# Kernel optimization log

Measured on AMD Instinct MI355X. Metric: run time of the kernel, lower is better.

## Reference

```python
import jax, jax.numpy as jnp
import numpy as np
import math

N_EMBD = 384
N_HEAD = 6
HEAD_DIM = N_EMBD // N_HEAD  # 64
EPS = 1e-5


def apply_rotary_emb(x, cos, sin):
    # x: [B, T, H, D]; cos/sin: [1, T, 1, D//2]
    d = x.shape[3] // 2
    x1, x2 = x[..., :d], x[..., d:]
    y1 = x1 * cos + x2 * sin
    y2 = -x1 * sin + x2 * cos
    return jnp.concatenate([y1, y2], axis=3).astype(x.dtype)


def rms_norm(x):
    # no learned gain, eps inside the sqrt's argument as in the torch code
    return x * jax.lax.rsqrt(jnp.mean(x * x, axis=-1, keepdims=True) + EPS)


def setup_inputs() -> dict:
    key = jax.random.key(0)
    ks = jax.random.split(key, 7)
    B, T = 8, 2048
    x = jax.random.normal(ks[0], (B, T, N_EMBD), dtype=jnp.float32)
    scale = 1.0 / math.sqrt(N_EMBD)
    Wq = jax.random.normal(ks[1], (N_EMBD, N_EMBD), dtype=jnp.float32) * scale
    Wk = jax.random.normal(ks[2], (N_EMBD, N_EMBD), dtype=jnp.float32) * scale
    Wv = jax.random.normal(ks[3], (N_EMBD, N_EMBD), dtype=jnp.float32) * scale
    Wo = jax.random.normal(ks[4], (N_EMBD, N_EMBD), dtype=jnp.float32) * scale
    # RoPE tables: true cos/sin of position*inv_freq
    half = HEAD_DIM // 2
    inv_freq = 1.0 / (10000.0 ** (jnp.arange(half, dtype=jnp.float32) / half))
    t = jnp.arange(T, dtype=jnp.float32)
    freqs = t[:, None] * inv_freq[None, :]  # [T, half]
    cos = jnp.cos(freqs)[None, :, None, :]  # [1, T, 1, half]
    sin = jnp.sin(freqs)[None, :, None, :]
    return {"x": x, "Wq": Wq, "Wk": Wk, "Wv": Wv, "Wo": Wo, "cos": cos, "sin": sin}


def reference(x, Wq, Wk, Wv, Wo, cos, sin):
    B, T, C = x.shape
    H, D = N_HEAD, HEAD_DIM
    # torch Linear: y = x @ W.T (weights stored [out, in])
    q = (x @ Wq.T).reshape(B, T, H, D)
    k = (x @ Wk.T).reshape(B, T, H, D)
    v = (x @ Wv.T).reshape(B, T, H, D)
    q = apply_rotary_emb(q, cos, sin)
    k = apply_rotary_emb(k, cos, sin)
    q = rms_norm(q)
    k = rms_norm(k)
    # attention: [B, H, T, T] scores, full softmax (no causal mask in source)
    att = jnp.einsum("bthd,bshd->bhts", q, k) * (1.0 / math.sqrt(D))
    att = jax.nn.softmax(att, axis=-1)
    y = jnp.einsum("bhts,bshd->bthd", att, v).reshape(B, T, C)
    return y @ Wo.T
```

## Files before the change

kernel.cpp:

```cpp
#include <hip/hip_runtime.h>
#include <hip/hip_bf16.h>
#include <stdint.h>

#define B_ 8
#define T_ 2048
#define C_ 384
#define H_ 6
#define D_ 64
#define M_ (B_*T_)

typedef unsigned short u16;
typedef unsigned int u32;
typedef __attribute__((ext_vector_type(8))) short short8;
typedef __attribute__((ext_vector_type(4))) float floatx4;
typedef __attribute__((ext_vector_type(16))) float floatx16;

#define QSCALE 0.18033688011112042f

__device__ __forceinline__ u16 f2b(float f) {
  union { float f; unsigned u; } x; x.f = f;
  unsigned r = x.u + 0x7fffu + ((x.u >> 16) & 1u);
  return (u16)(r >> 16);
}
__device__ __forceinline__ u32 pack_bf16(float a, float b) {
  union { __hip_bfloat162 h; u32 u; } x;
  x.h = __float22bfloat162_rn(float2{a, b});
  return x.u;
}
__device__ __forceinline__ uint4 pack8(const float4& lo, const float4& hi) {
  uint4 r;
  r.x = pack_bf16(lo.x, lo.y); r.y = pack_bf16(lo.z, lo.w);
  r.z = pack_bf16(hi.x, hi.y); r.w = pack_bf16(hi.z, hi.w);
  return r;
}

__device__ __forceinline__ void plswap(u32& a, u32& b) {
  asm("v_permlane32_swap_b32 %0, %1" : "+v"(a), "+v"(b));
}

__device__ __forceinline__ float fexp2(float x) {
#if __has_builtin(__builtin_amdgcn_exp2f)
  return __builtin_amdgcn_exp2f(x);
#else
  float r; asm("v_exp_f32 %0, %1" : "=v"(r) : "v"(x)); return r;
#endif
}

__device__ __forceinline__ u32 cvtpk(float a, float b) {
  u32 r; asm("v_cvt_pk_bf16_f32 %0, %1, %2" : "=v"(r) : "v"(a), "v"(b)); return r;
}

__device__ __forceinline__ void gl_lds16(const u16* g, u16* l) {
#if __has_builtin(__builtin_amdgcn_global_load_lds)
  __builtin_amdgcn_global_load_lds(
      (const __attribute__((address_space(1))) unsigned int*)g,
      (__attribute__((address_space(3))) unsigned int*)l,
      16, 0, 0);
#else
  *reinterpret_cast<uint4*>(l + (threadIdx.x & 63) * 8) =
      *reinterpret_cast<const uint4*>(g);
#endif
}

__device__ __forceinline__ void rawbar() {
  __builtin_amdgcn_sched_barrier(0);
  asm volatile("" ::: "memory");
  __builtin_amdgcn_s_barrier();
  asm volatile("" ::: "memory");
  __builtin_amdgcn_sched_barrier(0);
}

__global__ __launch_bounds__(256) void prep_bf16(
    const float* __restrict__ x,
    const float* __restrict__ wq, const float* __restrict__ wk,
    const float* __restrict__ wv, const float* __restrict__ wo,
    u16* __restrict__ xb,
    u16* __restrict__ wqb, u16* __restrict__ wkb,
    u16* __restrict__ wvb, u16* __restrict__ wob)
{
  const int c = blockIdx.x * 256 + threadIdx.x;
  const float* src;
  u16* dst;
  int off;
  if (c < 786432) {
    src = x; dst = xb; off = c;
  } else {
    int t = c - 786432;
    int wsel = t / 18432;
    off = t - wsel * 18432;
    src = (wsel == 0) ? wq : (wsel == 1) ? wk : (wsel == 2) ? wv : wo;
    dst = (wsel == 0) ? wqb : (wsel == 1) ? wkb : (wsel == 2) ? wvb : wob;
  }
  const float4* p = reinterpret_cast<const float4*>(src + (size_t)off * 8);
  float4 lo = p[0], hi = p[1];
  *reinterpret_cast<uint4*>(dst + (size_t)off * 8) = pack8(lo, hi);
}

#define QKV_SBUF 10240

__global__ __launch_bounds__(256, 3) void qkv_fused(
    const u16* __restrict__ Xb,
    const u16* __restrict__ Wqb, const u16* __restrict__ Wkb, const u16* __restrict__ Wvb,
    const float* __restrict__ cosb, const float* __restrict__ sinb,
    u16* __restrict__ Qo, u16* __restrict__ Ko, u16* __restrict__ Vto)
{
  __shared__ __align__(16) u16 smem[2 * QKV_SBUF];

  const int id = blockIdx.x;
  const int xcd = id & 7;
  const int s = id >> 3;
  const int mb = xcd * 16 + s / 6;
  const int hh = s % 6;
  const int m0 = mb * 128;
  const int n0 = hh * 64;

  const int tid = threadIdx.x;
  const int w = tid >> 6;
  const int lane = tid & 63;
  const int quad = lane >> 4;
  const int c = lane & 15;

  const u16* Wz[3] = {Wqb, Wkb, Wvb};

  floatx4 acc[3][2][4];
#pragma unroll
  for (int z = 0; z < 3; z++)
#pragma unroll
    for (int i = 0; i < 2; i++)
#pragma unroll
      for (int j = 0; j < 4; j++) acc[z][i][j] = (floatx4){0.f, 0.f, 0.f, 0.f};

  const int lrow = lane >> 2;
  const int lcol = (lane & 3) * 8;

  auto STAGE = [&](int bb, int k0) {
    u16* base = smem + bb * QKV_SBUF;
#pragma unroll
    for (int n = 0; n < 2; n++) {
      const int ch = w * 2 + n;
      gl_lds16(Xb + (size_t)(m0 + ch * 16 + lrow) * C_ + k0 + lcol, base + ch * 512);
    }
#pragma unroll
    for (int n = 0; n < 3; n++) {
      const int idx = w * 3 + n;
      const int z = idx >> 2;
      const int chz = idx & 3;
      gl_lds16(Wz[z] + (size_t)(n0 + chz * 16 + lrow) * C_ + k0 + lcol,
               base + 4096 + z * 2048 + chz * 512);
    }
  };

  STAGE(0, 0);
  STAGE(1, 32);

  for (int i = 0; i < 12; i++) {
    if (i < 11) asm volatile("s_waitcnt vmcnt(5)" ::: "memory");
    else        asm volatile("s_waitcnt vmcnt(0)" ::: "memory");
    rawbar();

    const u16* As = smem + (i & 1) * QKV_SBUF;
    const u16* Bs0 = As + 4096;
    __builtin_amdgcn_s_setprio(1);
    short8 af2[2];
#pragma unroll
    for (int mi = 0; mi < 2; mi++)
      af2[mi] = *reinterpret_cast<const short8*>(
          As + (w * 32 + mi * 16 + c) * 32 + quad * 8);
#pragma unroll
    for (int z = 0; z < 3; z++) {
#pragma unroll
      for (int ni = 0; ni < 4; ni++) {
        short8 bf = *reinterpret_cast<const short8*>(
            Bs0 + z * 2048 + (ni * 16 + c) * 32 + quad * 8);
#pragma unroll
        for (int mi = 0; mi < 2; mi++)
          acc[z][mi][ni] = __builtin_amdgcn_mfma_f32_16x16x32_bf16(af2[mi], bf, acc[z][mi][ni], 0, 0, 0);
      }
    }
    __builtin_amdgcn_s_setprio(0);

    rawbar();
    if (i + 2 < 12) STAGE(i & 1, (i + 2) * 32);
  }

  const int bb2 = m0 >> 11;
  const int tbase = m0 & (T_ - 1);

  {
    const size_t vbase = ((size_t)(bb2 * H_ + hh)) * D_ * T_;
#pragma unroll
    for (int mi = 0; mi < 2; mi++) {
      int t = tbase + w * 32 + mi * 16 + quad * 4;
#pragma unroll
      for (int ni = 0; ni < 4; ni++) {
        int d = ni * 16 + c;
        ushort4 pk;
        pk.x = f2b(acc[2][mi][ni][0]); pk.y = f2b(acc[2][mi][ni][1]);
        pk.z = f2b(acc[2][mi][ni][2]); pk.w = f2b(acc[2][mi][ni][3]);
        *reinterpret_cast<ushort4*>(Vto + vbase + (size_t)d * T_ + t) = pk;
      }
    }
  }

  u16* Ep = smem;
#pragma unroll
  for (int zz = 0; zz < 2; zz++) {
    __syncthreads();
#pragma unroll
    for (int mi = 0; mi < 2; mi++) {
      float ssr[4];
#pragma unroll
      for (int r = 0; r < 4; r++) {
        float s0 = acc[zz][mi][0][r], s1 = acc[zz][mi][1][r];
        float s2 = acc[zz][mi][2][r], s3 = acc[zz][mi][3][r];
        ssr[r] = s0 * s0 + s1 * s1 + s2 * s2 + s3 * s3;
      }
#pragma unroll
      for (int off = 1; off < 16; off <<= 1)
#pragma unroll
        for (int r = 0; r < 4; r++) ssr[r] += __shfl_xor(ssr[r], off, 64);
      int rowb = w * 32 + mi * 16 + quad * 4;
#pragma unroll
      for (int r = 0; r < 4; r++) {
        float scl = rsqrtf(ssr[r] * (1.0f / 64.0f) + 1e-5f);
        if (zz == 0) scl *= QSCALE;
        int t = tbase + rowb + r;
#pragma unroll
        for (int h2 = 0; h2 < 2; h2++) {
          float cs = cosb[t * 32 + h2 * 16 + c];
          float sn = sinb[t * 32 + h2 * 16 + c];
          float x1 = acc[zz][mi][h2][r];
          float x2 = acc[zz][mi][h2 + 2][r];
          Ep[(rowb + r) * 72 + h2 * 16 + c]       = f2b((x1 * cs + x2 * sn) * scl);
          Ep[(rowb + r) * 72 + (h2 + 2) * 16 + c] = f2b((x2 * cs - x1 * sn) * scl);
        }
      }
    }
    __syncthreads();
    {
      int row = tid >> 1, half = tid & 1;
      int t = tbase + row;
      u16* Og = (zz == 0) ? Qo : Ko;
      u16* dst = Og + (((size_t)(bb2 * H_ + hh)) * T_ + t) * D_ + half * 32;
#pragma unroll
      for (int i = 0; i < 4; i++)
        *reinterpret_cast<uint4*>(dst + i * 8) =
            *reinterpret_cast<const uint4*>(Ep + row * 72 + half * 32 + i * 8);
    }
  }
}

#define ATT_LDA 72
#define ATT_VOFF 4608
#define ATT_BUF 9216

__global__ __launch_bounds__(256, 3) void attn_mfma(
    const u16* __restrict__ Qg, const u16* __restrict__ Kg,
    const u16* __restrict__ Vtg, u16* __restrict__ Yg)
{
  __shared__ __align__(16) u16 smem[2 * ATT_BUF];

  const int tid = threadIdx.x;
  const int w = tid >> 6;
  const int lane = tid & 63;
  const int hi = lane >> 5;
  const int lq = lane & 31;

  const int id = blockIdx.x;
  const int xcd = id & 7;
  const int slot = id >> 3;
  const int bh = xcd * 6 + (slot >> 4);
  const int q0 = (slot & 15) * 128;

  const size_t baseQK = (size_t)bh * T_ * D_;
  const size_t baseV  = (size_t)bh * D_ * T_;

  short8 qf[4];
  {
    const u16* qp = Qg + baseQK + (size_t)(q0 + w * 32 + lq) * D_ + hi * 8;
#pragma unroll
    for (int d = 0; d < 4; d++)
      qf[d] = *reinterpret_cast<const short8*>(qp + d * 16);
  }

  floatx16 z16;
#pragma unroll
  for (int i = 0; i < 16; i++) z16[i] = 0.f;
  short8 vones;
#pragma unroll
  for (int i = 0; i < 8; i++) vones[i] = (short)0x3F80;

  const int sr = tid >> 2;
  const int sch = tid & 3;
  const int ko0 = sr * ATT_LDA + sch * 8;
  const int ko1 = sr * ATT_LDA + (sch + 4) * 8;
  const int vo0 = ATT_VOFF + ko0;
  const int vo1 = ATT_VOFF + ko1;
  const u16* kga = Kg + baseQK + (size_t)sr * D_ + sch * 8;
  const u16* vga = Vtg + baseV + (size_t)sr * T_ + sch * 8;

  uint4 ka = *reinterpret_cast<const uint4*>(kga);
  uint4 kb = *reinterpret_cast<const uint4*>(kga + 32);
  uint4 va = *reinterpret_cast<const uint4*>(vga);
  uint4 vb = *reinterpret_cast<const uint4*>(vga + 32);
  *reinterpret_cast<uint4*>(smem + ko0) = ka;
  *reinterpret_cast<uint4*>(smem + ko1) = kb;
  *reinterpret_cast<uint4*>(smem + vo0) = va;
  *reinterpret_cast<uint4*>(smem + vo1) = vb;
  const u16* kload = kga + (size_t)64 * D_;
  const u16* vload = vga + 64;
  ka = *reinterpret_cast<const uint4*>(kload);
  kb = *reinterpret_cast<const uint4*>(kload + 32);
  va = *reinterpret_cast<const uint4*>(vload);
  vb = *reinterpret_cast<const uint4*>(vload + 32);
  kload += (size_t)64 * D_;
  vload += 64;

  floatx16 o0 = z16, o1 = z16;
  floatx16 l_acc = z16;

  int koff[2][4], voff[2][4];
#pragma unroll
  for (int ds = 0; ds < 4; ds++) {
    const int xr = ds * 2 + hi;
    koff[0][ds] = lq * ATT_LDA + xr * 8;
    koff[1][ds] = (32 + lq) * ATT_LDA + xr * 8;
    voff[0][ds] = ATT_VOFF + lq * ATT_LDA + xr * 8;
    voff[1][ds] = ATT_VOFF + (32 + lq) * ATT_LDA + xr * 8;
  }

  for (int kt = 0; kt < 32; kt++) {
    __syncthreads();

    if (kt < 31) {
      u16* wb = smem + ((kt + 1) & 1) * ATT_BUF;
      *reinterpret_cast<uint4*>(wb + ko0) = ka;
      *reinterpret_cast<uint4*>(wb + ko1) = kb;
      *reinterpret_cast<uint4*>(wb + vo0) = va;
      *reinterpret_cast<uint4*>(wb + vo1) = vb;
      if (kt < 30) {
        ka = *reinterpret_cast<const uint4*>(kload);
        kb = *reinterpret_cast<const uint4*>(kload + 32);
        va = *reinterpret_cast<const uint4*>(vload);
        vb = *reinterpret_cast<const uint4*>(vload + 32);
        kload += (size_t)64 * D_;
        vload += 64;
      }
    }

    const u16* Ksb = smem + (kt & 1) * ATT_BUF;

    floatx16 st0, st1;
    __builtin_amdgcn_s_setprio(1);
    {
      short8 kf0 = *reinterpret_cast<const short8*>(Ksb + koff[0][0]);
      short8 kf1 = *reinterpret_cast<const short8*>(Ksb + koff[1][0]);
      st0 = __builtin_amdgcn_mfma_f32_32x32x16_bf16(kf0, qf[0], z16, 0, 0, 0);
      st1 = __builtin_amdgcn_mfma_f32_32x32x16_bf16(kf1, qf[0], z16, 0, 0, 0);
    }
#pragma unroll
    for (int ds = 1; ds < 4; ds++) {
      short8 kf0 = *reinterpret_cast<const short8*>(Ksb + koff[0][ds]);
      short8 kf1 = *reinterpret_cast<const short8*>(Ksb + koff[1][ds]);
      st0 = __builtin_amdgcn_mfma_f32_32x32x16_bf16(kf0, qf[ds], st0, 0, 0, 0);
      st1 = __builtin_amdgcn_mfma_f32_32x32x16_bf16(kf1, qf[ds], st1, 0, 0, 0);
    }
    __builtin_amdgcn_s_setprio(0);

#pragma unroll
    for (int r = 0; r < 16; r++) {
      st0[r] = fexp2(st0[r]);
      st1[r] = fexp2(st1[r]);
    }

    short8 pa[4];
#pragma unroll
    for (int ks = 0; ks < 4; ks++) {
      const floatx16& s = (ks < 2) ? st0 : st1;
      const int rb = (ks & 1) * 8;
      u32 ca = cvtpk(s[rb + 0], s[rb + 1]);
      u32 cb = cvtpk(s[rb + 2], s[rb + 3]);
      u32 cc = cvtpk(s[rb + 4], s[rb + 5]);
      u32 cd = cvtpk(s[rb + 6], s[rb + 7]);
      plswap(ca, cc);
      plswap(cb, cd);
      short8 pf;
      u32* pfu = reinterpret_cast<u32*>(&pf);
      pfu[0] = ca; pfu[1] = cb; pfu[2] = cc; pfu[3] = cd;
      pa[ks] = pf;
    }

    __builtin_amdgcn_s_setprio(1);
#pragma unroll
    for (int ks = 0; ks < 4; ks++) {
      short8 vf0 = *reinterpret_cast<const short8*>(Ksb + voff[0][ks]);
      short8 vf1 = *reinterpret_cast<const short8*>(Ksb + voff[1][ks]);
      o0 = __builtin_amdgcn_mfma_f32_32x32x16_bf16(pa[ks], vf0, o0, 0, 0, 0);
      o1 = __builtin_amdgcn_mfma_f32_32x32x16_bf16(pa[ks], vf1, o1, 0, 0, 0);
      l_acc = __builtin_amdgcn_mfma_f32_32x32x16_bf16(pa[ks], vones, l_acc, 0, 0, 0);
    }
    __builtin_amdgcn_s_setprio(0);
  }

  float invr[16];
#pragma unroll
  for (int r = 0; r < 16; r++) invr[r] = __builtin_amdgcn_rcpf(l_acc[r]);

  __syncthreads();
  u16* Ep = smem + w * (32 * 72);
#pragma unroll
  for (int nt = 0; nt < 2; nt++) {
    const floatx16& o = nt ? o1 : o0;
#pragma unroll
    for (int r = 0; r < 16; r++) {
      const int rl = (r & 3) + 8 * (r >> 2) + 4 * hi;
      Ep[rl * 72 + nt * 32 + lq] = f2b(o[r] * invr[r]);
    }
  }
  __syncthreads();
  {
    const int row = tid >> 1, half = tid & 1;
    const u16* src = smem + (row >> 5) * (32 * 72) + (row & 31) * 72 + half * 32;
    const int t = q0 + row;
    const int b = bh / H_, h = bh % H_;
    const size_t yi = ((size_t)b * T_ + t) * C_ + (size_t)h * 64 + half * 32;
#pragma unroll
    for (int i = 0; i < 4; i++)
      *reinterpret_cast<uint4*>(Yg + yi + i * 8) =
          *reinterpret_cast<const uint4*>(src + i * 8);
  }
}

#define OUT_SBUF 6144

__global__ __launch_bounds__(256, 4) void out_mfma(
    const u16* __restrict__ Xb, const u16* __restrict__ Wfb, float* __restrict__ Og)
{
  __shared__ __align__(16) u16 smem[17408];

  const int id = blockIdx.x;
  const int xcd = id & 7;
  const int s = id >> 3;
  const int m0 = (xcd * 16 + s / 6) * 128;
  const int n0 = (s % 6) * 64;

  const int tid = threadIdx.x;
  const int w = tid >> 6;
  const int lane = tid & 63;
  const int quad = lane >> 4;
  const int c = lane & 15;

  floatx4 acc[2][4];
#pragma unroll
  for (int i = 0; i < 2; i++)
#pragma unroll
    for (int j = 0; j < 4; j++) acc[i][j] = (floatx4){0.f, 0.f, 0.f, 0.f};

  const int lrow = lane >> 2;
  const int lcol = (lane & 3) * 8;

  auto STAGE = [&](int bb, int k0) {
    u16* base = smem + bb * OUT_SBUF;
#pragma unroll
    for (int n = 0; n < 2; n++) {
      const int ch = w * 2 + n;
      gl_lds16(Xb + (size_t)(m0 + ch * 16 + lrow) * C_ + k0 + lcol, base + ch * 512);
    }
    gl_lds16(Wfb + (size_t)(n0 + w * 16 + lrow) * C_ + k0 + lcol,
             base + 4096 + w * 512);
  };

  STAGE(0, 0);
  STAGE(1, 32);

  for (int i = 0; i < 12; i++) {
    if (i < 11) asm volatile("s_waitcnt vmcnt(3)" ::: "memory");
    else        asm volatile("s_waitcnt vmcnt(0)" ::: "memory");
    rawbar();

    const u16* As = smem + (i & 1) * OUT_SBUF;
    const u16* Bs = As + 4096;
    __builtin_amdgcn_s_setprio(1);
    short8 af[2], bf[4];
#pragma unroll
    for (int mi = 0; mi < 2; mi++)
      af[mi] = *reinterpret_cast<const short8*>(
          As + (w * 32 + mi * 16 + c) * 32 + quad * 8);
#pragma unroll
    for (int ni = 0; ni < 4; ni++)
      bf[ni] = *reinterpret_cast<const short8*>(
          Bs + (ni * 16 + c) * 32 + quad * 8);
#pragma unroll
    for (int mi = 0; mi < 2; mi++)
#pragma unroll
      for (int ni = 0; ni < 4; ni++)
        acc[mi][ni] = __builtin_amdgcn_mfma_f32_16x16x32_bf16(af[mi], bf[ni], acc[mi][ni], 0, 0, 0);
    __builtin_amdgcn_s_setprio(0);

    rawbar();
    if (i + 2 < 12) STAGE(i & 1, (i + 2) * 32);
  }

  __syncthreads();
  float* Ep = reinterpret_cast<float*>(smem) + w * (32 * 68);
#pragma unroll
  for (int mi = 0; mi < 2; mi++)
#pragma unroll
    for (int ni = 0; ni < 4; ni++) {
      int rw = mi * 16 + quad * 4;
      int col = ni * 16 + c;
#pragma unroll
      for (int r = 0; r < 4; r++)
        Ep[(rw + r) * 68 + col] = acc[mi][ni][r];
    }
  __syncthreads();
  {
    int rw2 = lane >> 1, half = lane & 1;
    const float* src = Ep + rw2 * 68 + half * 32;
    float* dst = Og + (size_t)(m0 + w * 32 + rw2) * C_ + n0 + half * 32;
#pragma unroll
    for (int i = 0; i < 8; i++)
      *reinterpret_cast<float4*>(dst + i * 4) =
          *reinterpret_cast<const float4*>(src + i * 4);
  }
}

extern "C" void kernel_launch(void* const* d_in, const int* in_sizes, int n_in,
                              void* d_out, int out_size, void* d_ws, size_t ws_size,
                              hipStream_t stream) {
  (void)in_sizes; (void)n_in; (void)out_size; (void)ws_size;
  const float* x    = (const float*)d_in[0];
  const float* Wq   = (const float*)d_in[1];
  const float* Wk   = (const float*)d_in[2];
  const float* Wv   = (const float*)d_in[3];
  const float* Wo   = (const float*)d_in[4];
  const float* cosb = (const float*)d_in[5];
  const float* sinb = (const float*)d_in[6];

  const size_t MC = (size_t)M_ * C_;
  u16* ws = (u16*)d_ws;
  u16* Q   = ws;
  u16* K   = Q + MC;
  u16* Vt  = K + MC;
  u16* Y   = Vt + MC;
  u16* Xb  = Y;
  u16* Wb  = Y + MC;
  u16* Wqb = Wb;
  u16* Wkb = Wb + 147456;
  u16* Wvb = Wb + 2 * 147456;
  u16* Wob = Wb + 3 * 147456;
  float* out = (float*)d_out;

  prep_bf16<<<3360, 256, 0, stream>>>(x, Wq, Wk, Wv, Wo, Xb, Wqb, Wkb, Wvb, Wob);

  qkv_fused<<<768, 256, 0, stream>>>(Xb, Wqb, Wkb, Wvb, cosb, sinb, Q, K, Vt);

  attn_mfma<<<768, 256, 0, stream>>>(Q, K, Vt, Y);

  out_mfma<<<768, 256, 0, stream>>>(Y, Wob, out);
}
```

Before: 192.2 us.

## Fuse x fp32-to-bf16 conversion into QKV GEMM register-staged A loads

Removes the separate conversion of activations x to bf16 in the prep kernel. The QKV GEMM now loads fp32 x straight into registers one stage ahead, converts it, and writes bf16 into LDS, while weights still use direct global-to-LDS loads. This drops a full write and reread of the bf16 x copy. In exchange each block reads twice the bytes for A (fp32 instead of bf16). The custom vmcnt/raw barrier pipelining is replaced by plain __syncthreads plus register prefetch.

```diff
diff --git a/kernel.cpp b/kernel.cpp
--- a/kernel.cpp
+++ b/kernel.cpp
@@ -70,27 +70,17 @@
   __builtin_amdgcn_sched_barrier(0);
 }
 
-__global__ __launch_bounds__(256) void prep_bf16(
-    const float* __restrict__ x,
+__global__ __launch_bounds__(256) void prep_w(
     const float* __restrict__ wq, const float* __restrict__ wk,
     const float* __restrict__ wv, const float* __restrict__ wo,
-    u16* __restrict__ xb,
     u16* __restrict__ wqb, u16* __restrict__ wkb,
     u16* __restrict__ wvb, u16* __restrict__ wob)
 {
   const int c = blockIdx.x * 256 + threadIdx.x;
-  const float* src;
-  u16* dst;
-  int off;
-  if (c < 786432) {
-    src = x; dst = xb; off = c;
-  } else {
-    int t = c - 786432;
-    int wsel = t / 18432;
-    off = t - wsel * 18432;
-    src = (wsel == 0) ? wq : (wsel == 1) ? wk : (wsel == 2) ? wv : wo;
-    dst = (wsel == 0) ? wqb : (wsel == 1) ? wkb : (wsel == 2) ? wvb : wob;
-  }
+  const int wsel = c / 18432;
+  const int off = c - wsel * 18432;
+  const float* src = (wsel == 0) ? wq : (wsel == 1) ? wk : (wsel == 2) ? wv : wo;
+  u16* dst = (wsel == 0) ? wqb : (wsel == 1) ? wkb : (wsel == 2) ? wvb : wob;
   const float4* p = reinterpret_cast<const float4*>(src + (size_t)off * 8);
   float4 lo = p[0], hi = p[1];
   *reinterpret_cast<uint4*>(dst + (size_t)off * 8) = pack8(lo, hi);
@@ -99,7 +89,7 @@
 #define QKV_SBUF 10240
 
 __global__ __launch_bounds__(256, 3) void qkv_fused(
-    const u16* __restrict__ Xb,
+    const float* __restrict__ Xf,
     const u16* __restrict__ Wqb, const u16* __restrict__ Wkb, const u16* __restrict__ Wvb,
     const float* __restrict__ cosb, const float* __restrict__ sinb,
     u16* __restrict__ Qo, u16* __restrict__ Ko, u16* __restrict__ Vto)
@@ -133,13 +123,27 @@
   const int lrow = lane >> 2;
   const int lcol = (lane & 3) * 8;
 
-  auto STAGE = [&](int bb, int k0) {
-    u16* base = smem + bb * QKV_SBUF;
+  float4 ar[2][2];
+  auto LOADA = [&](int k0) {
 #pragma unroll
     for (int n = 0; n < 2; n++) {
       const int ch = w * 2 + n;
-      gl_lds16(Xb + (size_t)(m0 + ch * 16 + lrow) * C_ + k0 + lcol, base + ch * 512);
-    }
+      const float* p = Xf + (size_t)(m0 + ch * 16 + lrow) * C_ + k0 + lcol;
+      ar[n][0] = *reinterpret_cast<const float4*>(p);
+      ar[n][1] = *reinterpret_cast<const float4*>(p + 4);
+    }
+  };
+  auto WRITEA = [&](int bb) {
+    u16* base = smem + bb * QKV_SBUF;
+#pragma unroll
+    for (int n = 0; n < 2; n++) {
+      const int ch = w * 2 + n;
+      *reinterpret_cast<uint4*>(base + ch * 512 + lrow * 32 + lcol) =
+          pack8(ar[n][0], ar[n][1]);
+    }
+  };
+  auto STAGEB = [&](int bb, int k0) {
+    u16* base = smem + bb * QKV_SBUF;
 #pragma unroll
     for (int n = 0; n < 3; n++) {
       const int idx = w * 3 + n;
@@ -150,14 +154,16 @@
     }
   };
 
-  STAGE(0, 0);
-  STAGE(1, 32);
+  LOADA(0);
+  WRITEA(0);
+  STAGEB(0, 0);
+  LOADA(32);
+  WRITEA(1);
+  STAGEB(1, 32);
+  LOADA(64);
+  __syncthreads();
 
   for (int i = 0; i < 12; i++) {
-    if (i < 11) asm volatile("s_waitcnt vmcnt(5)" ::: "memory");
-    else        asm volatile("s_waitcnt vmcnt(0)" ::: "memory");
-    rawbar();
-
     const u16* As = smem + (i & 1) * QKV_SBUF;
     const u16* Bs0 = As + 4096;
     __builtin_amdgcn_s_setprio(1);
@@ -179,8 +185,12 @@
     }
     __builtin_amdgcn_s_setprio(0);
 
-    rawbar();
-    if (i + 2 < 12) STAGE(i & 1, (i + 2) * 32);
+    __syncthreads();
+    if (i + 2 < 12) {
+      WRITEA(i & 1);
+      STAGEB(i & 1, (i + 2) * 32);
+      if (i + 3 < 12) LOADA((i + 3) * 32);
+    }
   }
 
   const int bb2 = m0 >> 11;
@@ -543,7 +553,6 @@
   u16* K   = Q + MC;
   u16* Vt  = K + MC;
   u16* Y   = Vt + MC;
-  u16* Xb  = Y;
   u16* Wb  = Y + MC;
   u16* Wqb = Wb;
   u16* Wkb = Wb + 147456;
@@ -551,9 +560,9 @@
   u16* Wob = Wb + 3 * 147456;
   float* out = (float*)d_out;
 
-  prep_bf16<<<3360, 256, 0, stream>>>(x, Wq, Wk, Wv, Wo, Xb, Wqb, Wkb, Wvb, Wob);
-
-  qkv_fused<<<768, 256, 0, stream>>>(Xb, Wqb, Wkb, Wvb, cosb, sinb, Q, K, Vt);
+  prep_w<<<288, 256, 0, stream>>>(Wq, Wk, Wv, Wo, Wqb, Wkb, Wvb, Wob);
+
+  qkv_fused<<<768, 256, 0, stream>>>(x, Wqb, Wkb, Wvb, cosb, sinb, Q, K, Vt);
 
   attn_mfma<<<768, 256, 0, stream>>>(Q, K, Vt, Y);
 
```

New measurement: 189.6 us, median of 2. About the same (-1.3%).
